# Optimization experiments

Measured on AMD Instinct MI355X. Metric: run time of the kernel, lower is better.

## Reference

```python
import jax, jax.numpy as jnp
import numpy as np

N = 1_000_000
D = 128
NUM_CLASSES = 1000


def setup_inputs() -> dict:
    key = jax.random.key(0)
    kx, ky = jax.random.split(key)
    X = jax.random.normal(kx, (N, D), dtype=jnp.float32)
    y = jax.random.randint(ky, (N,), 0, NUM_CLASSES, dtype=jnp.int32)
    return {"X": X, "y": y, "n_classes": NUM_CLASSES}


def reference(X, y, n_classes):
    # get_pca_output: [X_i ; global_mean ; per_class_mean[y_i]] per row.
    global_mean = jnp.mean(X, axis=0)  # [D]

    # _get_pca_mean_per_class as a fused scatter-mean (replaces python loop over classes)
    sums = jax.ops.segment_sum(X, y, num_segments=n_classes)          # [C, D]
    counts = jax.ops.segment_sum(jnp.ones((X.shape[0],), X.dtype), y,
                                 num_segments=n_classes)               # [C]
    has_members = counts > 0
    per_class_mean = jnp.where(
        has_members[:, None],
        sums / jnp.maximum(counts, 1.0)[:, None],
        global_mean[None, :],  # empty class falls back to global mean
    )  # [C, D]

    # row-wise gather + concat (replaces python loop over samples)
    lab = jnp.minimum(y, n_classes - 1)
    class_rows = per_class_mean[lab]                                   # [N, D]
    gmean_rows = jnp.broadcast_to(global_mean[None, :], X.shape)       # [N, D]
    return jnp.concatenate([X, gmean_rows, class_rows], axis=1)        # [N, 3D]
```

## Files before the change

### kernel.cpp

```cpp
#include <hip/hip_runtime.h>

static constexpr int D    = 128;
static constexpr int D2   = 64;
static constexpr int D4   = 32;
static constexpr int CMAX = 1024;
static constexpr int RCAP = 4096;

typedef float f32x2 __attribute__((ext_vector_type(2)));
typedef float f32x4 __attribute__((ext_vector_type(4)));

struct Ptrs {
  float* sums;
  int*   counts;
  int*   base;
  int*   cursor;
  float* gmean;
  float* cmean;
};
__device__ __forceinline__ Ptrs get_ptrs(void* ws) {
  Ptrs p;
  p.sums   = reinterpret_cast<float*>(ws);
  p.counts = reinterpret_cast<int*>(p.sums + (size_t)CMAX * D);
  p.base   = p.counts + CMAX;
  p.cursor = p.base + CMAX;
  p.gmean  = reinterpret_cast<float*>(p.cursor + CMAX);
  p.cmean  = p.gmean + D;
  return p;
}
static constexpr size_t FIXED_BYTES =
    ((size_t)CMAX * D + 3 * (size_t)CMAX + D + (size_t)CMAX * D) * 4;

__device__ __forceinline__ int clampc(int c, int C) {
  return min(max(c, 0), C - 1);
}


__global__ void zero_counts_kernel(void* ws) {
  get_ptrs(ws).counts[threadIdx.x] = 0;
}

__global__ void count_kernel(const int* __restrict__ y,
                             const int* __restrict__ ncp, void* ws, int n) {
  __shared__ int lh[CMAX];
  const int C = min(*ncp, CMAX);
  Ptrs p = get_ptrs(ws);
  for (int i = threadIdx.x; i < CMAX; i += blockDim.x) lh[i] = 0;
  __syncthreads();
  for (int i = blockIdx.x * blockDim.x + threadIdx.x; i < n;
       i += gridDim.x * blockDim.x)
    atomicAdd(&lh[clampc(y[i], C)], 1);
  __syncthreads();
  for (int c = threadIdx.x; c < CMAX; c += blockDim.x)
    if (lh[c]) atomicAdd(&p.counts[c], lh[c]);
}

__global__ void scan_kernel(void* ws) {
  Ptrs p = get_ptrs(ws);
  __shared__ int s[CMAX];
  const int t  = threadIdx.x;
  const int my = p.counts[t];
  s[t] = my;
  __syncthreads();
  for (int off = 1; off < CMAX; off <<= 1) {
    const int add = (t >= off) ? s[t - off] : 0;
    __syncthreads();
    s[t] += add;
    __syncthreads();
  }
  const int excl = s[t] - my;
  p.base[t]   = excl;
  p.cursor[t] = excl;
}

__global__ void scatter_kernel(const int* __restrict__ y,
                               const int* __restrict__ ncp, void* ws,
                               int* __restrict__ rowid, int n, int rpb) {
  __shared__ int lcnt[CMAX];
  __shared__ int lbase[CMAX];
  const int C = min(*ncp, CMAX);
  Ptrs p = get_ptrs(ws);
  for (int i = threadIdx.x; i < CMAX; i += blockDim.x) lcnt[i] = 0;
  __syncthreads();
  const int r0 = blockIdx.x * rpb;
  const int r1 = min(r0 + rpb, n);
  for (int i = r0 + threadIdx.x; i < r1; i += blockDim.x)
    atomicAdd(&lcnt[clampc(y[i], C)], 1);
  __syncthreads();
  for (int c = threadIdx.x; c < CMAX; c += blockDim.x) {
    const int k = lcnt[c];
    lbase[c] = k ? atomicAdd(&p.cursor[c], k) : 0;
    lcnt[c]  = 0;
  }
  __syncthreads();
  for (int i = r0 + threadIdx.x; i < r1; i += blockDim.x) {
    const int c   = clampc(y[i], C);
    const int pos = lbase[c] + atomicAdd(&lcnt[c], 1);
    rowid[pos] = i;
  }
}

__global__ __launch_bounds__(512) void gather_kernel(
    const float* __restrict__ X, const int* __restrict__ ncp, void* ws,
    const int* __restrict__ rowid, float* __restrict__ out) {
  __shared__ int   lrid[RCAP];
  __shared__ f32x2 red[8][D2];
  const int C = min(*ncp, CMAX);
  Ptrs p = get_ptrs(ws);
  const int c   = blockIdx.x;
  const int cnt = (c < C) ? p.counts[c] : 0;
  const int b   = (c < C) ? p.base[c] : 0;
  const int m   = min(cnt, RCAP);
  for (int i = threadIdx.x; i < m; i += blockDim.x) lrid[i] = rowid[b + i];
  __syncthreads();

  const int d2  = threadIdx.x & (D2 - 1);
  const int sub = threadIdx.x >> 6;
  const f32x2* X2 = reinterpret_cast<const f32x2*>(X);
  f32x2*       o2 = reinterpret_cast<f32x2*>(out);
  f32x2 acc = {0.f, 0.f};
  int i = sub;
  for (; i + 24 < m; i += 32) {
    const int ra = lrid[i], rb = lrid[i + 8], rc = lrid[i + 16], rd = lrid[i + 24];
    const f32x2 va = __builtin_nontemporal_load(&X2[(size_t)ra * D2 + d2]);
    const f32x2 vb = __builtin_nontemporal_load(&X2[(size_t)rb * D2 + d2]);
    const f32x2 vc = __builtin_nontemporal_load(&X2[(size_t)rc * D2 + d2]);
    const f32x2 vd = __builtin_nontemporal_load(&X2[(size_t)rd * D2 + d2]);
    __builtin_nontemporal_store(va, &o2[(size_t)ra * 192 + d2]);
    __builtin_nontemporal_store(vb, &o2[(size_t)rb * 192 + d2]);
    __builtin_nontemporal_store(vc, &o2[(size_t)rc * 192 + d2]);
    __builtin_nontemporal_store(vd, &o2[(size_t)rd * 192 + d2]);
    acc += va + vb + vc + vd;
  }
  for (; i < m; i += 8) {
    const int r = lrid[i];
    const f32x2 v = __builtin_nontemporal_load(&X2[(size_t)r * D2 + d2]);
    __builtin_nontemporal_store(v, &o2[(size_t)r * 192 + d2]);
    acc += v;
  }
  for (int k = RCAP + sub; k < cnt; k += 8) {
    const int r = rowid[b + k];
    const f32x2 v = __builtin_nontemporal_load(&X2[(size_t)r * D2 + d2]);
    __builtin_nontemporal_store(v, &o2[(size_t)r * 192 + d2]);
    acc += v;
  }
  red[sub][d2] = acc;
  __syncthreads();
  if (sub == 0) {
    f32x2 t = acc;
#pragma unroll
    for (int k = 1; k < 8; ++k) t += red[k][d2];
    reinterpret_cast<f32x2*>(p.sums)[(size_t)c * D2 + d2] = t;
  }
}


__global__ void zero_sums_counts_kernel(void* ws) {
  int* w = reinterpret_cast<int*>(ws);
  const int total = CMAX * D + CMAX;
  for (int i = blockIdx.x * blockDim.x + threadIdx.x; i < total;
       i += gridDim.x * blockDim.x)
    w[i] = 0;
}

__global__ void accum_atomic_kernel(const float* __restrict__ X,
                                    const int* __restrict__ y,
                                    const int* __restrict__ ncp, void* ws,
                                    int n) {
  const int C = min(*ncp, CMAX);
  Ptrs p = get_ptrs(ws);
  const int g    = threadIdx.x >> 5;
  const int lane = threadIdx.x & 31;
  const long long stride = (long long)gridDim.x * 8;
  for (long long row = (long long)blockIdx.x * 8 + g; row < n; row += stride) {
    const int c = clampc(y[row], C);
    const float4 v = reinterpret_cast<const float4*>(X)[row * D4 + lane];
    float* s = p.sums + (size_t)c * D + lane * 4;
    unsafeAtomicAdd(s + 0, v.x);
    unsafeAtomicAdd(s + 1, v.y);
    unsafeAtomicAdd(s + 2, v.z);
    unsafeAtomicAdd(s + 3, v.w);
    if (lane == 0) atomicAdd(p.counts + c, 1);
  }
}


__global__ void gmean_kernel(void* ws, const int* __restrict__ ncp, float invN) {
  const int C = min(*ncp, CMAX);
  Ptrs p = get_ptrs(ws);
  __shared__ float red[8][D];
  const int d = threadIdx.x & (D - 1);
  const int g = threadIdx.x >> 7;
  float acc = 0.f;
  for (int c = g; c < C; c += 8) acc += p.sums[c * D + d];
  red[g][d] = acc;
  __syncthreads();
  if (g == 0) {
    float t = 0.f;
#pragma unroll
    for (int k = 0; k < 8; ++k) t += red[k][d];
    p.gmean[d] = t * invN;
  }
}

__global__ void cmean_kernel(void* ws, const int* __restrict__ ncp) {
  const int C = min(*ncp, CMAX);
  Ptrs p = get_ptrs(ws);
  const int total = C * D;
  for (int i = blockIdx.x * blockDim.x + threadIdx.x; i < total;
       i += gridDim.x * blockDim.x) {
    const int cnt = p.counts[i >> 7];
    p.cmean[i] = (cnt > 0) ? (p.sums[i] / (float)cnt) : p.gmean[i & (D - 1)];
  }
}


__global__ __launch_bounds__(256) void write_thirds_kernel(
    const int* __restrict__ y, const int* __restrict__ ncp,
    float* __restrict__ out, void* ws, int n) {
  const int C = min(*ncp, CMAX);
  Ptrs p = get_ptrs(ws);
  const f32x4* gm4 = reinterpret_cast<const f32x4*>(p.gmean);
  const f32x4* cm4 = reinterpret_cast<const f32x4*>(p.cmean);
  f32x4*       o4  = reinterpret_cast<f32x4*>(out);
  const int j  = threadIdx.x & 63;
  const int lr = threadIdx.x >> 6;
  f32x4 vg;
  if (j < D4) vg = gm4[j];
  const long long rpi = (long long)gridDim.x * 4;
  for (long long row = (long long)blockIdx.x * 4 + lr; row < n; row += rpi) {
    f32x4 v;
    if (j < D4) {
      v = vg;
    } else {
      const int c = clampc(y[row], C);
      v = cm4[(size_t)c * D4 + (j - D4)];
    }
    __builtin_nontemporal_store(v, &o4[(size_t)row * 96 + D4 + j]);
  }
}

__global__ __launch_bounds__(384) void write_full_kernel(
    const float* __restrict__ X, const int* __restrict__ y,
    const int* __restrict__ ncp, float* __restrict__ out, void* ws, int n) {
  const int C = min(*ncp, CMAX);
  Ptrs p = get_ptrs(ws);
  const f32x4* X4  = reinterpret_cast<const f32x4*>(X);
  const f32x4* gm4 = reinterpret_cast<const f32x4*>(p.gmean);
  const f32x4* cm4 = reinterpret_cast<const f32x4*>(p.cmean);
  f32x4*       o4  = reinterpret_cast<f32x4*>(out);
  const int j  = threadIdx.x % 96;
  const int lr = threadIdx.x / 96;
  f32x4 vg;
  if (j >= D4 && j < 2 * D4) vg = gm4[j - D4];
  const long long rpi = (long long)gridDim.x * 4;
  for (long long row = (long long)blockIdx.x * 4 + lr; row < n; row += rpi) {
    f32x4 v;
    if (j < D4) {
      v = __builtin_nontemporal_load(&X4[(size_t)row * D4 + j]);
    } else if (j < 2 * D4) {
      v = vg;
    } else {
      const int c = clampc(y[row], C);
      v = cm4[(size_t)c * D4 + (j - 2 * D4)];
    }
    __builtin_nontemporal_store(v, &o4[(size_t)row * 96 + j]);
  }
}

extern "C" void kernel_launch(void* const* d_in, const int* in_sizes, int n_in,
                              void* d_out, int out_size, void* d_ws,
                              size_t ws_size, hipStream_t stream) {
  const float* X   = reinterpret_cast<const float*>(d_in[0]);
  const int*   y   = reinterpret_cast<const int*>(d_in[1]);
  const int*   ncp = reinterpret_cast<const int*>(d_in[2]);
  float*       out = reinterpret_cast<float*>(d_out);
  const int n = in_sizes[1];
  const float invN = 1.0f / (float)n;

  const size_t need = FIXED_BYTES + (size_t)n * sizeof(int);
  if (ws_size >= need) {
    int* rowid = reinterpret_cast<int*>((char*)d_ws + FIXED_BYTES);
    const int rpb = (n + 63) / 64;
    zero_counts_kernel<<<1, CMAX, 0, stream>>>(d_ws);
    count_kernel<<<256, 256, 0, stream>>>(y, ncp, d_ws, n);
    scan_kernel<<<1, CMAX, 0, stream>>>(d_ws);
    scatter_kernel<<<64, 256, 0, stream>>>(y, ncp, d_ws, rowid, n, rpb);
    gather_kernel<<<CMAX, 512, 0, stream>>>(X, ncp, d_ws, rowid, out);
    gmean_kernel<<<1, 1024, 0, stream>>>(d_ws, ncp, invN);
    cmean_kernel<<<512, 256, 0, stream>>>(d_ws, ncp);
    write_thirds_kernel<<<2048, 256, 0, stream>>>(y, ncp, out, d_ws, n);
  } else {
    zero_sums_counts_kernel<<<256, 256, 0, stream>>>(d_ws);
    accum_atomic_kernel<<<4096, 256, 0, stream>>>(X, y, ncp, d_ws, n);
    gmean_kernel<<<1, 1024, 0, stream>>>(d_ws, ncp, invN);
    cmean_kernel<<<512, 256, 0, stream>>>(d_ws, ncp);
    write_full_kernel<<<2048, 384, 0, stream>>>(X, y, ncp, out, d_ws, n);
  }
}
```

Before: 498.5 us.

## Split per-class gather across blocks with atomic sums and parallelize global mean

The gather kernel now launches SPLIT blocks per class, each copying a quarter of that class's rows with 16-byte vector loads and stores. Each block adds its partial class sum into the sums buffer with atomics, so that buffer is now zeroed up front. The single-block global-mean reduction becomes an 8-block partial pass plus a small final kernel. The scatter and write_thirds kernels get larger blocks. The aim is more parallelism and occupancy in the memory-bound gather than one block per class gave, at the cost of float atomics (order-dependent rounding) and extra launches.

After: 471.8 us. -5.3%, faster.

```diff
diff --git a/kernel.cpp b/kernel.cpp
--- a/kernel.cpp
+++ b/kernel.cpp
@@ -1,10 +1,10 @@
 #include <hip/hip_runtime.h>
 
-static constexpr int D    = 128;
-static constexpr int D2   = 64;
-static constexpr int D4   = 32;
-static constexpr int CMAX = 1024;
-static constexpr int RCAP = 4096;
+static constexpr int D     = 128;
+static constexpr int D4    = 32;
+static constexpr int CMAX  = 1024;
+static constexpr int SPLIT = 4;
+static constexpr int RCAP  = 2048;
 
 typedef float f32x2 __attribute__((ext_vector_type(2)));
 typedef float f32x4 __attribute__((ext_vector_type(4)));
@@ -16,6 +16,7 @@
   int*   cursor;
   float* gmean;
   float* cmean;
+  float* gpart;
 };
 __device__ __forceinline__ Ptrs get_ptrs(void* ws) {
   Ptrs p;
@@ -25,19 +26,24 @@
   p.cursor = p.base + CMAX;
   p.gmean  = reinterpret_cast<float*>(p.cursor + CMAX);
   p.cmean  = p.gmean + D;
+  p.gpart  = p.cmean + (size_t)CMAX * D;
   return p;
 }
 static constexpr size_t FIXED_BYTES =
-    ((size_t)CMAX * D + 3 * (size_t)CMAX + D + (size_t)CMAX * D) * 4;
+    ((size_t)CMAX * D + 3 * (size_t)CMAX + D + (size_t)CMAX * D + 8 * D) * 4;
 
 __device__ __forceinline__ int clampc(int c, int C) {
   return min(max(c, 0), C - 1);
 }
 
-
-__global__ void zero_counts_kernel(void* ws) {
-  get_ptrs(ws).counts[threadIdx.x] = 0;
-}
+__global__ void zero_kernel(void* ws) {
+  int* w = reinterpret_cast<int*>(ws);
+  const int total = CMAX * D + CMAX;
+  for (int i = blockIdx.x * blockDim.x + threadIdx.x; i < total;
+       i += gridDim.x * blockDim.x)
+    w[i] = 0;
+}
+
 
 __global__ void count_kernel(const int* __restrict__ y,
                              const int* __restrict__ ncp, void* ws, int n) {
@@ -72,9 +78,9 @@
   p.cursor[t] = excl;
 }
 
-__global__ void scatter_kernel(const int* __restrict__ y,
-                               const int* __restrict__ ncp, void* ws,
-                               int* __restrict__ rowid, int n, int rpb) {
+__global__ __launch_bounds__(1024) void scatter_kernel(
+    const int* __restrict__ y, const int* __restrict__ ncp, void* ws,
+    int* __restrict__ rowid, int n, int rpb) {
   __shared__ int lcnt[CMAX];
   __shared__ int lbase[CMAX];
   const int C = min(*ncp, CMAX);
@@ -103,64 +109,71 @@
     const float* __restrict__ X, const int* __restrict__ ncp, void* ws,
     const int* __restrict__ rowid, float* __restrict__ out) {
   __shared__ int   lrid[RCAP];
-  __shared__ f32x2 red[8][D2];
-  const int C = min(*ncp, CMAX);
-  Ptrs p = get_ptrs(ws);
-  const int c   = blockIdx.x;
+  __shared__ f32x4 red[16][32];
+  const int C = min(*ncp, CMAX);
+  Ptrs p = get_ptrs(ws);
+  const int c = blockIdx.x & (CMAX - 1);
+  const int s = blockIdx.x >> 10;
   const int cnt = (c < C) ? p.counts[c] : 0;
-  const int b   = (c < C) ? p.base[c] : 0;
-  const int m   = min(cnt, RCAP);
-  for (int i = threadIdx.x; i < m; i += blockDim.x) lrid[i] = rowid[b + i];
-  __syncthreads();
-
-  const int d2  = threadIdx.x & (D2 - 1);
-  const int sub = threadIdx.x >> 6;
-  const f32x2* X2 = reinterpret_cast<const f32x2*>(X);
-  f32x2*       o2 = reinterpret_cast<f32x2*>(out);
-  f32x2 acc = {0.f, 0.f};
-  int i = sub;
-  for (; i + 24 < m; i += 32) {
-    const int ra = lrid[i], rb = lrid[i + 8], rc = lrid[i + 16], rd = lrid[i + 24];
-    const f32x2 va = __builtin_nontemporal_load(&X2[(size_t)ra * D2 + d2]);
-    const f32x2 vb = __builtin_nontemporal_load(&X2[(size_t)rb * D2 + d2]);
-    const f32x2 vc = __builtin_nontemporal_load(&X2[(size_t)rc * D2 + d2]);
-    const f32x2 vd = __builtin_nontemporal_load(&X2[(size_t)rd * D2 + d2]);
-    __builtin_nontemporal_store(va, &o2[(size_t)ra * 192 + d2]);
-    __builtin_nontemporal_store(vb, &o2[(size_t)rb * 192 + d2]);
-    __builtin_nontemporal_store(vc, &o2[(size_t)rc * 192 + d2]);
-    __builtin_nontemporal_store(vd, &o2[(size_t)rd * 192 + d2]);
+  if (cnt == 0) return;
+  const int q  = (cnt + SPLIT - 1) / SPLIT;
+  const int i0 = s * q;
+  if (i0 >= cnt) return;
+  const int i1 = min(i0 + q, cnt);
+  const int b  = p.base[c];
+  const int m  = i1 - i0;
+  const int sm = min(m, RCAP);
+  for (int k = threadIdx.x; k < sm; k += blockDim.x) lrid[k] = rowid[b + i0 + k];
+  __syncthreads();
+
+  const int lane = threadIdx.x & 63;
+  const int d4   = lane & 31;
+  const int half = lane >> 5;
+  const int sub  = threadIdx.x >> 6;
+  const int slot = sub * 2 + half;
+  const f32x4* X4 = reinterpret_cast<const f32x4*>(X);
+  f32x4*       o4 = reinterpret_cast<f32x4*>(out);
+  f32x4 acc = {0.f, 0.f, 0.f, 0.f};
+  int lk = slot;
+  for (; lk + 48 < sm; lk += 64) {
+    const int ra = lrid[lk], rb = lrid[lk + 16], rc = lrid[lk + 32],
+              rd = lrid[lk + 48];
+    const f32x4 va = __builtin_nontemporal_load(&X4[(size_t)ra * D4 + d4]);
+    const f32x4 vb = __builtin_nontemporal_load(&X4[(size_t)rb * D4 + d4]);
+    const f32x4 vc = __builtin_nontemporal_load(&X4[(size_t)rc * D4 + d4]);
+    const f32x4 vd = __builtin_nontemporal_load(&X4[(size_t)rd * D4 + d4]);
+    __builtin_nontemporal_store(va, &o4[(size_t)ra * 96 + d4]);
+    __builtin_nontemporal_store(vb, &o4[(size_t)rb * 96 + d4]);
+    __builtin_nontemporal_store(vc, &o4[(size_t)rc * 96 + d4]);
+    __builtin_nontemporal_store(vd, &o4[(size_t)rd * 96 + d4]);
     acc += va + vb + vc + vd;
   }
-  for (; i < m; i += 8) {
-    const int r = lrid[i];
-    const f32x2 v = __builtin_nontemporal_load(&X2[(size_t)r * D2 + d2]);
-    __builtin_nontemporal_store(v, &o2[(size_t)r * 192 + d2]);
+  for (; lk < sm; lk += 16) {
+    const int r = lrid[lk];
+    const f32x4 v = __builtin_nontemporal_load(&X4[(size_t)r * D4 + d4]);
+    __builtin_nontemporal_store(v, &o4[(size_t)r * 96 + d4]);
     acc += v;
   }
-  for (int k = RCAP + sub; k < cnt; k += 8) {
+  for (int k = i0 + RCAP + slot; k < i1; k += 16) {
     const int r = rowid[b + k];
-    const f32x2 v = __builtin_nontemporal_load(&X2[(size_t)r * D2 + d2]);
-    __builtin_nontemporal_store(v, &o2[(size_t)r * 192 + d2]);
+    const f32x4 v = __builtin_nontemporal_load(&X4[(size_t)r * D4 + d4]);
+    __builtin_nontemporal_store(v, &o4[(size_t)r * 96 + d4]);
     acc += v;
   }
-  red[sub][d2] = acc;
-  __syncthreads();
-  if (sub == 0) {
-    f32x2 t = acc;
+  red[slot][d4] = acc;
+  __syncthreads();
+  if (threadIdx.x < 32) {
+    f32x4 t = red[0][threadIdx.x];
 #pragma unroll
-    for (int k = 1; k < 8; ++k) t += red[k][d2];
-    reinterpret_cast<f32x2*>(p.sums)[(size_t)c * D2 + d2] = t;
-  }
-}
-
-
-__global__ void zero_sums_counts_kernel(void* ws) {
-  int* w = reinterpret_cast<int*>(ws);
-  const int total = CMAX * D + CMAX;
-  for (int i = blockIdx.x * blockDim.x + threadIdx.x; i < total;
-       i += gridDim.x * blockDim.x)
-    w[i] = 0;
-}
+    for (int k = 1; k < 16; ++k) t += red[k][threadIdx.x];
+    float* dst = p.sums + (size_t)c * D + threadIdx.x * 4;
+    unsafeAtomicAdd(dst + 0, t.x);
+    unsafeAtomicAdd(dst + 1, t.y);
+    unsafeAtomicAdd(dst + 2, t.z);
+    unsafeAtomicAdd(dst + 3, t.w);
+  }
+}
+
 
 __global__ void accum_atomic_kernel(const float* __restrict__ X,
                                     const int* __restrict__ y,
@@ -174,32 +187,32 @@
   for (long long row = (long long)blockIdx.x * 8 + g; row < n; row += stride) {
     const int c = clampc(y[row], C);
     const float4 v = reinterpret_cast<const float4*>(X)[row * D4 + lane];
-    float* s = p.sums + (size_t)c * D + lane * 4;
-    unsafeAtomicAdd(s + 0, v.x);
-    unsafeAtomicAdd(s + 1, v.y);
-    unsafeAtomicAdd(s + 2, v.z);
-    unsafeAtomicAdd(s + 3, v.w);
+    float* sp = p.sums + (size_t)c * D + lane * 4;
+    unsafeAtomicAdd(sp + 0, v.x);
+    unsafeAtomicAdd(sp + 1, v.y);
+    unsafeAtomicAdd(sp + 2, v.z);
+    unsafeAtomicAdd(sp + 3, v.w);
     if (lane == 0) atomicAdd(p.counts + c, 1);
   }
 }
 
 
-__global__ void gmean_kernel(void* ws, const int* __restrict__ ncp, float invN) {
-  const int C = min(*ncp, CMAX);
-  Ptrs p = get_ptrs(ws);
-  __shared__ float red[8][D];
-  const int d = threadIdx.x & (D - 1);
-  const int g = threadIdx.x >> 7;
-  float acc = 0.f;
-  for (int c = g; c < C; c += 8) acc += p.sums[c * D + d];
-  red[g][d] = acc;
-  __syncthreads();
-  if (g == 0) {
-    float t = 0.f;
+__global__ void gpart_kernel(void* ws) {
+  Ptrs p = get_ptrs(ws);
+  const int d = threadIdx.x;
+  const int g = blockIdx.x;
+  float t = 0.f;
+  for (int c = g * 128; c < (g + 1) * 128; ++c) t += p.sums[(size_t)c * D + d];
+  p.gpart[g * D + d] = t;
+}
+
+__global__ void gmean_final_kernel(void* ws, float invN) {
+  Ptrs p = get_ptrs(ws);
+  const int d = threadIdx.x;
+  float t = 0.f;
 #pragma unroll
-    for (int k = 0; k < 8; ++k) t += red[k][d];
-    p.gmean[d] = t * invN;
-  }
+  for (int g = 0; g < 8; ++g) t += p.gpart[g * D + d];
+  p.gmean[d] = t * invN;
 }
 
 __global__ void cmean_kernel(void* ws, const int* __restrict__ ncp) {
@@ -214,7 +227,7 @@
 }
 
 
-__global__ __launch_bounds__(256) void write_thirds_kernel(
+__global__ __launch_bounds__(512) void write_thirds_kernel(
     const int* __restrict__ y, const int* __restrict__ ncp,
     float* __restrict__ out, void* ws, int n) {
   const int C = min(*ncp, CMAX);
@@ -226,8 +239,8 @@
   const int lr = threadIdx.x >> 6;
   f32x4 vg;
   if (j < D4) vg = gm4[j];
-  const long long rpi = (long long)gridDim.x * 4;
-  for (long long row = (long long)blockIdx.x * 4 + lr; row < n; row += rpi) {
+  const long long rpi = (long long)gridDim.x * 8;
+  for (long long row = (long long)blockIdx.x * 8 + lr; row < n; row += rpi) {
     f32x4 v;
     if (j < D4) {
       v = vg;
@@ -281,18 +294,20 @@
   if (ws_size >= need) {
     int* rowid = reinterpret_cast<int*>((char*)d_ws + FIXED_BYTES);
     const int rpb = (n + 63) / 64;
-    zero_counts_kernel<<<1, CMAX, 0, stream>>>(d_ws);
+    zero_kernel<<<128, 256, 0, stream>>>(d_ws);
     count_kernel<<<256, 256, 0, stream>>>(y, ncp, d_ws, n);
     scan_kernel<<<1, CMAX, 0, stream>>>(d_ws);
-    scatter_kernel<<<64, 256, 0, stream>>>(y, ncp, d_ws, rowid, n, rpb);
-    gather_kernel<<<CMAX, 512, 0, stream>>>(X, ncp, d_ws, rowid, out);
-    gmean_kernel<<<1, 1024, 0, stream>>>(d_ws, ncp, invN);
+    scatter_kernel<<<64, 1024, 0, stream>>>(y, ncp, d_ws, rowid, n, rpb);
+    gather_kernel<<<SPLIT * CMAX, 512, 0, stream>>>(X, ncp, d_ws, rowid, out);
+    gpart_kernel<<<8, 128, 0, stream>>>(d_ws);
+    gmean_final_kernel<<<1, 128, 0, stream>>>(d_ws, invN);
     cmean_kernel<<<512, 256, 0, stream>>>(d_ws, ncp);
-    write_thirds_kernel<<<2048, 256, 0, stream>>>(y, ncp, out, d_ws, n);
+    write_thirds_kernel<<<3072, 512, 0, stream>>>(y, ncp, out, d_ws, n);
   } else {
-    zero_sums_counts_kernel<<<256, 256, 0, stream>>>(d_ws);
+    zero_kernel<<<128, 256, 0, stream>>>(d_ws);
     accum_atomic_kernel<<<4096, 256, 0, stream>>>(X, y, ncp, d_ws, n);
-    gmean_kernel<<<1, 1024, 0, stream>>>(d_ws, ncp, invN);
+    gpart_kernel<<<8, 128, 0, stream>>>(d_ws);
+    gmean_final_kernel<<<1, 128, 0, stream>>>(d_ws, invN);
     cmean_kernel<<<512, 256, 0, stream>>>(d_ws, ncp);
     write_full_kernel<<<2048, 384, 0, stream>>>(X, y, ncp, out, d_ws, n);
   }
```
